# Optimization experiments

Measured on AMD Instinct MI355X. Metric: run time of the kernel, lower is better.

The kernel has to match this reference:

```python
import jax, jax.numpy as jnp
import numpy as np

T, K, E, H, I = 2048, 8, 32, 1024, 768


def setup_inputs() -> dict:
    key = jax.random.key(0)
    k0, k1, k2, k3, k4, k5 = jax.random.split(key, 6)
    sh = 1.0 / np.sqrt(H).astype(np.float32)
    si = 1.0 / np.sqrt(I).astype(np.float32)
    return {
        "hidden_states": jax.random.normal(k0, (T, H), jnp.float32),
        "top_k_index": jax.random.randint(k1, (T, K), 0, E),
        "top_k_weights": jax.random.uniform(k2, (T, K), jnp.float32),
        "gate_proj": jax.random.normal(k3, (E, I, H), jnp.float32) * sh,
        "up_proj": jax.random.normal(k4, (E, I, H), jnp.float32) * sh,
        "down_proj": jax.random.normal(k5, (E, H, I), jnp.float32) * si,
    }


def reference(hidden_states, top_k_index, top_k_weights, gate_proj, up_proj, down_proj):
    # Tokens not routed to expert e get combine weight 0, so summing the
    # weighted per-expert outputs over all experts reproduces the original
    # gather -> SwiGLU MLP -> scale -> index_add_ exactly (duplicated expert
    # hits within a token's top-k sum, matching repeated index_add_).
    n_tok = hidden_states.shape[0]
    n_exp = gate_proj.shape[0]
    combine = jnp.zeros((n_tok, n_exp), hidden_states.dtype)
    combine = combine.at[jnp.arange(n_tok)[:, None], top_k_index].add(top_k_weights)

    def body(acc, xs):
        g_w, u_w, d_w, w_e = xs  # g_w,u_w: [I,H]; d_w: [H,I]; w_e: [T]
        h = jax.nn.silu(hidden_states @ g_w.T) * (hidden_states @ u_w.T)  # [T,I]
        y = h @ d_w.T  # [T,H]
        return acc + y * w_e[:, None], None

    out, _ = jax.lax.scan(
        body,
        jnp.zeros_like(hidden_states),
        (gate_proj, up_proj, down_proj, combine.T),
    )
    return out
```

## Files before the change

### kernel.cpp

```cpp
#include <hip/hip_runtime.h>

#define T_TOK 2048
#define TOPK  8
#define NEXP  32
#define HDIM  1024
#define IDIM  768
#define NPAIR (T_TOK * TOPK)
#define BM 128
#define BK 32
#define MT_MAX (NPAIR / BM + NEXP)

typedef __attribute__((ext_vector_type(8))) short short8;
typedef __attribute__((ext_vector_type(4))) float f32x4;

__device__ __forceinline__ unsigned short f2bf(float f) {
    unsigned x = __float_as_uint(f);
    unsigned r = x + 0x7fffu + ((x >> 16) & 1u);
    return (unsigned short)(r >> 16);
}
__device__ __forceinline__ float bf2f(unsigned short u) {
    return __uint_as_float(((unsigned)u) << 16);
}

__device__ __forceinline__ void gl_lds16(const unsigned short* g, void* l) {
    __builtin_amdgcn_global_load_lds((const __attribute__((address_space(1))) void*)g,
                                     (__attribute__((address_space(3))) void*)l, 16, 0, 0);
}

__device__ __forceinline__ int mt_swz(int bx) {
    return ((bx >> 4) << 4) | ((bx & 7) << 1) | ((bx >> 3) & 1);
}

#define VMCNT(n) asm volatile("s_waitcnt vmcnt(" #n ")" ::: "memory")
#define BARRIER  __builtin_amdgcn_s_barrier()

__global__ void k_conv2(const float* __restrict__ src0, const float* __restrict__ src1,
                        unsigned short* __restrict__ dst, int n4each) {
    int i = blockIdx.x * 256 + threadIdx.x;
    const float* s = (i < n4each) ? src0 : src1;
    int j = (i < n4each) ? i : i - n4each;
    if (i < 2 * n4each) {
        float4 v = ((const float4*)s)[j];
        ushort4 o;
        o.x = f2bf(v.x); o.y = f2bf(v.y); o.z = f2bf(v.z); o.w = f2bf(v.w);
        ((ushort4*)dst)[i] = o;
    }
}

__global__ void k_conv(const float* __restrict__ src, unsigned short* __restrict__ dst, int n4) {
    int i = blockIdx.x * 256 + threadIdx.x;
    if (i < n4) {
        float4 v = ((const float4*)src)[i];
        ushort4 o;
        o.x = f2bf(v.x); o.y = f2bf(v.y); o.z = f2bf(v.z); o.w = f2bf(v.w);
        ((ushort4*)dst)[i] = o;
    }
}

__global__ void k_init(int* counts) {
    if (threadIdx.x < NEXP) counts[threadIdx.x] = 0;
}

__global__ void k_hist(const int* __restrict__ idx, int* __restrict__ counts) {
    int p = blockIdx.x * 256 + threadIdx.x;
    atomicAdd(&counts[idx[p]], 1);
}

__global__ void k_scan(const int* __restrict__ counts, int* __restrict__ offsets,
                       int* __restrict__ mtb, int* __restrict__ cursor) {
    if (threadIdx.x == 0) {
        int tot = 0, mt = 0;
        for (int e = 0; e < NEXP; ++e) {
            offsets[e] = tot; mtb[e] = mt;
            tot += counts[e];
            mt += (counts[e] + BM - 1) / BM;
        }
        offsets[NEXP] = tot; mtb[NEXP] = mt;
    }
    if (threadIdx.x < NEXP) cursor[threadIdx.x] = 0;
}

__global__ void k_scatter(const int* __restrict__ idx, int* __restrict__ cursor,
                          const int* __restrict__ offsets, int* __restrict__ pair_token,
                          int* __restrict__ pair_slot) {
    int p = blockIdx.x * 256 + threadIdx.x;
    int e = idx[p];
    int pos = atomicAdd(&cursor[e], 1);
    int slot = offsets[e] + pos;
    pair_token[slot] = p >> 3;
    pair_slot[p] = slot;
}

__global__ __launch_bounds__(256, 2) void k_gateup(
    const unsigned short* __restrict__ hid_bf, const unsigned short* __restrict__ gate_bf,
    const unsigned short* __restrict__ up_bf, const int* __restrict__ pair_token,
    const int* __restrict__ offsets, const int* __restrict__ mtb,
    unsigned short* __restrict__ h_mid)
{
    __shared__ short8 sBuf[2][1536];
    __shared__ int sInfo[4];
    int tid = threadIdx.x;
    int mt = mt_swz(blockIdx.x);
    if (tid == 0 && mt >= mtb[NEXP]) sInfo[0] = -1;
    if (tid < NEXP) {
        int lo = mtb[tid], hi = mtb[tid + 1];
        if (lo <= mt && mt < hi) {
            sInfo[0] = tid; sInfo[1] = offsets[tid];
            sInfo[2] = offsets[tid + 1] - offsets[tid];
            sInfo[3] = (mt - lo) * BM;
        }
    }
    __syncthreads();
    int e = sInfo[0];
    if (e < 0) return;
    int off = sInfo[1], Me = sInfo[2], mrow0 = sInfo[3];
    int n0 = blockIdx.y * 128;

    int wave = tid >> 6, lane = tid & 63, quad = lane >> 4, l16 = lane & 15;

    int m0 = wave * 32 + l16, m1 = m0 + 16;
    int rp0 = mrow0 + m0, rp1 = mrow0 + m1;
    int tok0 = (rp0 < Me) ? pair_token[off + rp0] : 0;
    int tok1 = (rp1 < Me) ? pair_token[off + rp1] : 0;
    const unsigned short* aG0 = hid_bf + (size_t)tok0 * HDIM + quad * 8;
    const unsigned short* aG1 = hid_bf + (size_t)tok1 * HDIM + quad * 8;
    const unsigned short* gG0 = gate_bf + ((size_t)e * IDIM + n0 + m0) * HDIM + quad * 8;
    const unsigned short* gG1 = gate_bf + ((size_t)e * IDIM + n0 + m1) * HDIM + quad * 8;
    const unsigned short* uG0 = up_bf + ((size_t)e * IDIM + n0 + m0) * HDIM + quad * 8;
    const unsigned short* uG1 = up_bf + ((size_t)e * IDIM + n0 + m1) * HDIM + quad * 8;
    const int dA = wave * 128;
    const int dG = 512 + wave * 128;
    const int dU = 1024 + wave * 128;

    int wm = (wave & 1) * 64, wn = (wave >> 1) * 64;
    int aBase = (wm >> 4) * 64 + quad * 16 + l16;
    int bBase = (wn >> 4) * 64 + quad * 16 + l16;

    f32x4 zero = {0.f, 0.f, 0.f, 0.f};
    f32x4 accg[4][4], accu[4][4];
#pragma unroll
    for (int i = 0; i < 4; ++i)
#pragma unroll
        for (int j = 0; j < 4; ++j) { accg[i][j] = zero; accu[i][j] = zero; }

#define STAGE_GU(b, k0) do { \
        short8* nb_ = &sBuf[b][0]; \
        gl_lds16(aG0 + (k0), (void*)(nb_ + dA));      gl_lds16(aG1 + (k0), (void*)(nb_ + dA + 64)); \
        gl_lds16(gG0 + (k0), (void*)(nb_ + dG));      gl_lds16(gG1 + (k0), (void*)(nb_ + dG + 64)); \
        gl_lds16(uG0 + (k0), (void*)(nb_ + dU));      gl_lds16(uG1 + (k0), (void*)(nb_ + dU + 64)); \
    } while (0)

#define COMP_GU(b) do { \
        const short8* cb_ = &sBuf[b][0]; \
        short8 af_[4]; \
        _Pragma("unroll") for (int fm = 0; fm < 4; ++fm) af_[fm] = cb_[aBase + fm * 64]; \
        _Pragma("unroll") for (int fn = 0; fn < 4; ++fn) { \
            short8 bg_ = cb_[512 + bBase + fn * 64]; \
            short8 bu_ = cb_[1024 + bBase + fn * 64]; \
            _Pragma("unroll") for (int fm = 0; fm < 4; ++fm) { \
                accg[fm][fn] = __builtin_amdgcn_mfma_f32_16x16x32_bf16(af_[fm], bg_, accg[fm][fn], 0, 0, 0); \
                accu[fm][fn] = __builtin_amdgcn_mfma_f32_16x16x32_bf16(af_[fm], bu_, accu[fm][fn], 0, 0, 0); \
            } \
        } \
    } while (0)

    STAGE_GU(0, 0);
    STAGE_GU(1, BK);
#pragma unroll 1
    for (int tt = 0; tt < HDIM / BK - 2; tt += 2) {
        VMCNT(6); BARRIER; COMP_GU(0); BARRIER; STAGE_GU(0, (tt + 2) * BK);
        VMCNT(6); BARRIER; COMP_GU(1); BARRIER; STAGE_GU(1, (tt + 3) * BK);
    }
    VMCNT(6); BARRIER; COMP_GU(0);
    VMCNT(0); BARRIER; COMP_GU(1);

#pragma unroll
    for (int fm = 0; fm < 4; ++fm)
#pragma unroll
        for (int fn = 0; fn < 4; ++fn)
#pragma unroll
            for (int r = 0; r < 4; ++r) {
                int mloc = wm + fm * 16 + quad * 4 + r;
                int prow = mrow0 + mloc;
                if (prow < Me) {
                    int col = n0 + wn + fn * 16 + l16;
                    float g = accg[fm][fn][r], u = accu[fm][fn][r];
                    float h = g / (1.f + __expf(-g)) * u;
                    h_mid[(size_t)(off + prow) * IDIM + col] = f2bf(h);
                }
            }
}

__global__ __launch_bounds__(256, 2) void k_down(
    const unsigned short* __restrict__ h_mid, const unsigned short* __restrict__ down_bf,
    const int* __restrict__ offsets, const int* __restrict__ mtb,
    unsigned short* __restrict__ y_pair)
{
    __shared__ short8 sBuf[2][1536];
    __shared__ int sInfo[4];
    int tid = threadIdx.x;
    int mt = mt_swz(blockIdx.x);
    if (tid == 0 && mt >= mtb[NEXP]) sInfo[0] = -1;
    if (tid < NEXP) {
        int lo = mtb[tid], hi = mtb[tid + 1];
        if (lo <= mt && mt < hi) {
            sInfo[0] = tid; sInfo[1] = offsets[tid];
            sInfo[2] = offsets[tid + 1] - offsets[tid];
            sInfo[3] = (mt - lo) * BM;
        }
    }
    __syncthreads();
    int e = sInfo[0];
    if (e < 0) return;
    int off = sInfo[1], Me = sInfo[2], mrow0 = sInfo[3];
    int n0 = blockIdx.y * 256;

    int wave = tid >> 6, lane = tid & 63, quad = lane >> 4, l16 = lane & 15;

    int m0 = wave * 32 + l16, m1 = m0 + 16;
    int rp0 = mrow0 + m0; if (rp0 >= Me) rp0 = 0;
    int rp1 = mrow0 + m1; if (rp1 >= Me) rp1 = 0;
    const unsigned short* aG0 = h_mid + (size_t)(off + rp0) * IDIM + quad * 8;
    const unsigned short* aG1 = h_mid + (size_t)(off + rp1) * IDIM + quad * 8;
    const unsigned short* bG0 = down_bf + ((size_t)e * HDIM + n0 + wave * 64 + l16) * IDIM + quad * 8;
    const unsigned short* bG1 = bG0 + (size_t)16 * IDIM;
    const unsigned short* bG2 = bG0 + (size_t)32 * IDIM;
    const unsigned short* bG3 = bG0 + (size_t)48 * IDIM;
    const int dA = wave * 128;
    const int dB = 512 + wave * 256;

    int wm = (wave & 1) * 64, wn = (wave >> 1) * 128;
    int aBase = (wm >> 4) * 64 + quad * 16 + l16;
    int bBase = (wn >> 4) * 64 + quad * 16 + l16;

    f32x4 zero = {0.f, 0.f, 0.f, 0.f};
    f32x4 acc[4][8];
#pragma unroll
    for (int i = 0; i < 4; ++i)
#pragma unroll
        for (int j = 0; j < 8; ++j) acc[i][j] = zero;

#define STAGE_DN(b, k0) do { \
        short8* nb_ = &sBuf[b][0]; \
        gl_lds16(aG0 + (k0), (void*)(nb_ + dA));       gl_lds16(aG1 + (k0), (void*)(nb_ + dA + 64)); \
        gl_lds16(bG0 + (k0), (void*)(nb_ + dB));       gl_lds16(bG1 + (k0), (void*)(nb_ + dB + 64)); \
        gl_lds16(bG2 + (k0), (void*)(nb_ + dB + 128)); gl_lds16(bG3 + (k0), (void*)(nb_ + dB + 192)); \
    } while (0)

#define COMP_DN(b) do { \
        const short8* cb_ = &sBuf[b][0]; \
        short8 af_[4]; \
        _Pragma("unroll") for (int fm = 0; fm < 4; ++fm) af_[fm] = cb_[aBase + fm * 64]; \
        _Pragma("unroll") for (int fn = 0; fn < 8; ++fn) { \
            short8 bb_ = cb_[512 + bBase + fn * 64]; \
            _Pragma("unroll") for (int fm = 0; fm < 4; ++fm) \
                acc[fm][fn] = __builtin_amdgcn_mfma_f32_16x16x32_bf16(af_[fm], bb_, acc[fm][fn], 0, 0, 0); \
        } \
    } while (0)

    STAGE_DN(0, 0);
    STAGE_DN(1, BK);
#pragma unroll 1
    for (int tt = 0; tt < IDIM / BK - 2; tt += 2) {
        VMCNT(6); BARRIER; COMP_DN(0); BARRIER; STAGE_DN(0, (tt + 2) * BK);
        VMCNT(6); BARRIER; COMP_DN(1); BARRIER; STAGE_DN(1, (tt + 3) * BK);
    }
    VMCNT(6); BARRIER; COMP_DN(0);
    VMCNT(0); BARRIER; COMP_DN(1);

#pragma unroll
    for (int fm = 0; fm < 4; ++fm)
#pragma unroll
        for (int fn = 0; fn < 8; ++fn)
#pragma unroll
            for (int r = 0; r < 4; ++r) {
                int mloc = wm + fm * 16 + quad * 4 + r;
                int prow = mrow0 + mloc;
                if (prow < Me) {
                    int col = n0 + wn + fn * 16 + l16;
                    y_pair[(size_t)(off + prow) * HDIM + col] = f2bf(acc[fm][fn][r]);
                }
            }
}

__global__ void k_reduce(const unsigned short* __restrict__ y_pair,
                         const int* __restrict__ pair_slot,
                         const float* __restrict__ topw, float* __restrict__ out)
{
    int t = blockIdx.x;
    __shared__ int ss[TOPK];
    __shared__ float sw[TOPK];
    if (threadIdx.x < TOPK) {
        ss[threadIdx.x] = pair_slot[t * TOPK + threadIdx.x];
        sw[threadIdx.x] = topw[t * TOPK + threadIdx.x];
    }
    __syncthreads();
    int c = threadIdx.x * 4;
    float a0 = 0.f, a1 = 0.f, a2 = 0.f, a3 = 0.f;
    for (int k = 0; k < TOPK; ++k) {
        const unsigned short* yr = y_pair + (size_t)ss[k] * HDIM + c;
        uint2 v = *(const uint2*)yr;
        float w = sw[k];
        a0 += w * bf2f((unsigned short)(v.x & 0xffff));
        a1 += w * bf2f((unsigned short)(v.x >> 16));
        a2 += w * bf2f((unsigned short)(v.y & 0xffff));
        a3 += w * bf2f((unsigned short)(v.y >> 16));
    }
    float4 o = {a0, a1, a2, a3};
    *(float4*)(out + (size_t)t * HDIM + c) = o;
}

extern "C" void kernel_launch(void* const* d_in, const int* in_sizes, int n_in,
                              void* d_out, int out_size, void* d_ws, size_t ws_size,
                              hipStream_t stream) {
    (void)in_sizes; (void)n_in; (void)out_size; (void)ws_size;
    const float* hidden = (const float*)d_in[0];
    const int*   tki    = (const int*)d_in[1];
    const float* tkw    = (const float*)d_in[2];
    const float* gate   = (const float*)d_in[3];
    const float* up     = (const float*)d_in[4];
    const float* down   = (const float*)d_in[5];
    float* out = (float*)d_out;

    char* w = (char*)d_ws;
    unsigned short* h_mid   = (unsigned short*)w;
    unsigned short* hid_bf  = (unsigned short*)(w + 25165824);
    unsigned short* gate_bf = (unsigned short*)(w + 29360128);
    unsigned short* up_bf   = (unsigned short*)(w + 79691776);
    unsigned short* down_bf = gate_bf;
    unsigned short* y_pair  = up_bf;
    int* ib = (int*)(w + 130023424);
    int* pair_token = ib;
    int* pair_slot  = ib + NPAIR;
    int* counts     = ib + 2 * NPAIR;
    int* cursor     = counts + NEXP;
    int* offsets    = cursor + NEXP;
    int* mtb        = offsets + NEXP + 1;

    const int W4 = NEXP * IDIM * HDIM / 4;
    const int H4 = T_TOK * HDIM / 4;

    k_init<<<1, 64, 0, stream>>>(counts);
    k_hist<<<NPAIR / 256, 256, 0, stream>>>(tki, counts);
    k_scan<<<1, 64, 0, stream>>>(counts, offsets, mtb, cursor);
    k_scatter<<<NPAIR / 256, 256, 0, stream>>>(tki, cursor, offsets, pair_token, pair_slot);

    k_conv<<<(H4 + 255) / 256, 256, 0, stream>>>(hidden, hid_bf, H4);
    k_conv2<<<(2 * W4 + 255) / 256, 256, 0, stream>>>(gate, up, gate_bf, W4);

    k_gateup<<<dim3(MT_MAX, IDIM / 128), 256, 0, stream>>>(hid_bf, gate_bf, up_bf,
                                                           pair_token, offsets, mtb, h_mid);

    k_conv<<<(W4 + 255) / 256, 256, 0, stream>>>(down, down_bf, W4);

    k_down<<<dim3(MT_MAX, HDIM / 256), 256, 0, stream>>>(h_mid, down_bf, offsets, mtb, y_pair);
    k_reduce<<<T_TOK, 256, 0, stream>>>(y_pair, pair_slot, tkw, out);
}
```

Before: 545.5 us.

## Drop LDS staging in MoE GEMMs; load MFMA fragments directly from global

Both grouped GEMM kernels stop staging tiles through shared memory with global_load_lds and barriers. Each wave now loads its own bf16 fragments straight from global memory into registers with a two-slot register double buffer. The output tiles are halved (gate/up 128x64, down 128x128) and occupancy is raised to 3 blocks per SIMD group. This removes LDS traffic and barrier stalls, but each wave now loads its own copy of tiles that were shared in LDS, so global and L2 traffic goes up and the 16-byte-per-lane loads are less coalesced.

```diff
diff --git a/kernel.cpp b/kernel.cpp
--- a/kernel.cpp
+++ b/kernel.cpp
@@ -22,17 +22,9 @@
     return __uint_as_float(((unsigned)u) << 16);
 }
 
-__device__ __forceinline__ void gl_lds16(const unsigned short* g, void* l) {
-    __builtin_amdgcn_global_load_lds((const __attribute__((address_space(1))) void*)g,
-                                     (__attribute__((address_space(3))) void*)l, 16, 0, 0);
-}
-
 __device__ __forceinline__ int mt_swz(int bx) {
     return ((bx >> 4) << 4) | ((bx & 7) << 1) | ((bx >> 3) & 1);
 }
-
-#define VMCNT(n) asm volatile("s_waitcnt vmcnt(" #n ")" ::: "memory")
-#define BARRIER  __builtin_amdgcn_s_barrier()
 
 __global__ void k_conv2(const float* __restrict__ src0, const float* __restrict__ src1,
                         unsigned short* __restrict__ dst, int n4each) {
@@ -91,13 +83,12 @@
     pair_slot[p] = slot;
 }
 
-__global__ __launch_bounds__(256, 2) void k_gateup(
+__global__ __launch_bounds__(256, 3) void k_gateup(
     const unsigned short* __restrict__ hid_bf, const unsigned short* __restrict__ gate_bf,
     const unsigned short* __restrict__ up_bf, const int* __restrict__ pair_token,
     const int* __restrict__ offsets, const int* __restrict__ mtb,
     unsigned short* __restrict__ h_mid)
 {
-    __shared__ short8 sBuf[2][1536];
     __shared__ int sInfo[4];
     int tid = threadIdx.x;
     int mt = mt_swz(blockIdx.x);
@@ -114,70 +105,66 @@
     int e = sInfo[0];
     if (e < 0) return;
     int off = sInfo[1], Me = sInfo[2], mrow0 = sInfo[3];
-    int n0 = blockIdx.y * 128;
+    int n0 = blockIdx.y * 64;
 
     int wave = tid >> 6, lane = tid & 63, quad = lane >> 4, l16 = lane & 15;
-
-    int m0 = wave * 32 + l16, m1 = m0 + 16;
-    int rp0 = mrow0 + m0, rp1 = mrow0 + m1;
-    int tok0 = (rp0 < Me) ? pair_token[off + rp0] : 0;
-    int tok1 = (rp1 < Me) ? pair_token[off + rp1] : 0;
-    const unsigned short* aG0 = hid_bf + (size_t)tok0 * HDIM + quad * 8;
-    const unsigned short* aG1 = hid_bf + (size_t)tok1 * HDIM + quad * 8;
-    const unsigned short* gG0 = gate_bf + ((size_t)e * IDIM + n0 + m0) * HDIM + quad * 8;
-    const unsigned short* gG1 = gate_bf + ((size_t)e * IDIM + n0 + m1) * HDIM + quad * 8;
-    const unsigned short* uG0 = up_bf + ((size_t)e * IDIM + n0 + m0) * HDIM + quad * 8;
-    const unsigned short* uG1 = up_bf + ((size_t)e * IDIM + n0 + m1) * HDIM + quad * 8;
-    const int dA = wave * 128;
-    const int dG = 512 + wave * 128;
-    const int dU = 1024 + wave * 128;
-
-    int wm = (wave & 1) * 64, wn = (wave >> 1) * 64;
-    int aBase = (wm >> 4) * 64 + quad * 16 + l16;
-    int bBase = (wn >> 4) * 64 + quad * 16 + l16;
+    int wm = (wave & 1) * 64, wn = (wave >> 1) * 32;
+
+    const unsigned short* aP[4];
+#pragma unroll
+    for (int fm = 0; fm < 4; ++fm) {
+        int rp = mrow0 + wm + fm * 16 + l16;
+        int tok = pair_token[off + ((rp < Me) ? rp : (Me - 1))];
+        aP[fm] = hid_bf + (size_t)tok * HDIM + quad * 8;
+    }
+    const unsigned short* gP[2];
+    const unsigned short* uP[2];
+#pragma unroll
+    for (int fn = 0; fn < 2; ++fn) {
+        size_t row = (size_t)e * IDIM + n0 + wn + fn * 16 + l16;
+        gP[fn] = gate_bf + row * HDIM + quad * 8;
+        uP[fn] = up_bf   + row * HDIM + quad * 8;
+    }
 
     f32x4 zero = {0.f, 0.f, 0.f, 0.f};
-    f32x4 accg[4][4], accu[4][4];
+    f32x4 accg[4][2], accu[4][2];
 #pragma unroll
     for (int i = 0; i < 4; ++i)
 #pragma unroll
-        for (int j = 0; j < 4; ++j) { accg[i][j] = zero; accu[i][j] = zero; }
-
-#define STAGE_GU(b, k0) do { \
-        short8* nb_ = &sBuf[b][0]; \
-        gl_lds16(aG0 + (k0), (void*)(nb_ + dA));      gl_lds16(aG1 + (k0), (void*)(nb_ + dA + 64)); \
-        gl_lds16(gG0 + (k0), (void*)(nb_ + dG));      gl_lds16(gG1 + (k0), (void*)(nb_ + dG + 64)); \
-        gl_lds16(uG0 + (k0), (void*)(nb_ + dU));      gl_lds16(uG1 + (k0), (void*)(nb_ + dU + 64)); \
+        for (int j = 0; j < 2; ++j) { accg[i][j] = zero; accu[i][j] = zero; }
+
+    short8 A0[4], G0[2], U0[2], A1[4], G1[2], U1[2];
+
+#define LDALL_GU(A_, G_, U_, kk) do { \
+        _Pragma("unroll") for (int i = 0; i < 4; ++i) A_[i] = *(const short8*)(aP[i] + (kk)); \
+        _Pragma("unroll") for (int i = 0; i < 2; ++i) G_[i] = *(const short8*)(gP[i] + (kk)); \
+        _Pragma("unroll") for (int i = 0; i < 2; ++i) U_[i] = *(const short8*)(uP[i] + (kk)); \
     } while (0)
 
-#define COMP_GU(b) do { \
-        const short8* cb_ = &sBuf[b][0]; \
-        short8 af_[4]; \
-        _Pragma("unroll") for (int fm = 0; fm < 4; ++fm) af_[fm] = cb_[aBase + fm * 64]; \
-        _Pragma("unroll") for (int fn = 0; fn < 4; ++fn) { \
-            short8 bg_ = cb_[512 + bBase + fn * 64]; \
-            short8 bu_ = cb_[1024 + bBase + fn * 64]; \
+#define FMA_GU(A_, G_, U_) do { \
+        _Pragma("unroll") for (int fn = 0; fn < 2; ++fn) \
             _Pragma("unroll") for (int fm = 0; fm < 4; ++fm) { \
-                accg[fm][fn] = __builtin_amdgcn_mfma_f32_16x16x32_bf16(af_[fm], bg_, accg[fm][fn], 0, 0, 0); \
-                accu[fm][fn] = __builtin_amdgcn_mfma_f32_16x16x32_bf16(af_[fm], bu_, accu[fm][fn], 0, 0, 0); \
+                accg[fm][fn] = __builtin_amdgcn_mfma_f32_16x16x32_bf16(A_[fm], G_[fn], accg[fm][fn], 0, 0, 0); \
+                accu[fm][fn] = __builtin_amdgcn_mfma_f32_16x16x32_bf16(A_[fm], U_[fn], accu[fm][fn], 0, 0, 0); \
             } \
-        } \
     } while (0)
 
-    STAGE_GU(0, 0);
-    STAGE_GU(1, BK);
+    LDALL_GU(A0, G0, U0, 0);
 #pragma unroll 1
-    for (int tt = 0; tt < HDIM / BK - 2; tt += 2) {
-        VMCNT(6); BARRIER; COMP_GU(0); BARRIER; STAGE_GU(0, (tt + 2) * BK);
-        VMCNT(6); BARRIER; COMP_GU(1); BARRIER; STAGE_GU(1, (tt + 3) * BK);
-    }
-    VMCNT(6); BARRIER; COMP_GU(0);
-    VMCNT(0); BARRIER; COMP_GU(1);
+    for (int k0 = 0; k0 < HDIM - 64; k0 += 64) {
+        LDALL_GU(A1, G1, U1, k0 + 32);
+        FMA_GU(A0, G0, U0);
+        LDALL_GU(A0, G0, U0, k0 + 64);
+        FMA_GU(A1, G1, U1);
+    }
+    LDALL_GU(A1, G1, U1, HDIM - 32);
+    FMA_GU(A0, G0, U0);
+    FMA_GU(A1, G1, U1);
 
 #pragma unroll
     for (int fm = 0; fm < 4; ++fm)
 #pragma unroll
-        for (int fn = 0; fn < 4; ++fn)
+        for (int fn = 0; fn < 2; ++fn)
 #pragma unroll
             for (int r = 0; r < 4; ++r) {
                 int mloc = wm + fm * 16 + quad * 4 + r;
@@ -191,12 +178,11 @@
             }
 }
 
-__global__ __launch_bounds__(256, 2) void k_down(
+__global__ __launch_bounds__(256, 3) void k_down(
     const unsigned short* __restrict__ h_mid, const unsigned short* __restrict__ down_bf,
     const int* __restrict__ offsets, const int* __restrict__ mtb,
     unsigned short* __restrict__ y_pair)
 {
-    __shared__ short8 sBuf[2][1536];
     __shared__ int sInfo[4];
     int tid = threadIdx.x;
     int mt = mt_swz(blockIdx.x);
@@ -213,65 +199,59 @@
     int e = sInfo[0];
     if (e < 0) return;
     int off = sInfo[1], Me = sInfo[2], mrow0 = sInfo[3];
-    int n0 = blockIdx.y * 256;
+    int n0 = blockIdx.y * 128;
 
     int wave = tid >> 6, lane = tid & 63, quad = lane >> 4, l16 = lane & 15;
-
-    int m0 = wave * 32 + l16, m1 = m0 + 16;
-    int rp0 = mrow0 + m0; if (rp0 >= Me) rp0 = 0;
-    int rp1 = mrow0 + m1; if (rp1 >= Me) rp1 = 0;
-    const unsigned short* aG0 = h_mid + (size_t)(off + rp0) * IDIM + quad * 8;
-    const unsigned short* aG1 = h_mid + (size_t)(off + rp1) * IDIM + quad * 8;
-    const unsigned short* bG0 = down_bf + ((size_t)e * HDIM + n0 + wave * 64 + l16) * IDIM + quad * 8;
-    const unsigned short* bG1 = bG0 + (size_t)16 * IDIM;
-    const unsigned short* bG2 = bG0 + (size_t)32 * IDIM;
-    const unsigned short* bG3 = bG0 + (size_t)48 * IDIM;
-    const int dA = wave * 128;
-    const int dB = 512 + wave * 256;
-
-    int wm = (wave & 1) * 64, wn = (wave >> 1) * 128;
-    int aBase = (wm >> 4) * 64 + quad * 16 + l16;
-    int bBase = (wn >> 4) * 64 + quad * 16 + l16;
+    int wm = (wave & 1) * 64, wn = (wave >> 1) * 64;
+
+    const unsigned short* aP[4];
+#pragma unroll
+    for (int fm = 0; fm < 4; ++fm) {
+        int rp = mrow0 + wm + fm * 16 + l16;
+        if (rp >= Me) rp = Me - 1;
+        aP[fm] = h_mid + (size_t)(off + rp) * IDIM + quad * 8;
+    }
+    const unsigned short* bP[4];
+#pragma unroll
+    for (int fn = 0; fn < 4; ++fn)
+        bP[fn] = down_bf + ((size_t)e * HDIM + n0 + wn + fn * 16 + l16) * IDIM + quad * 8;
 
     f32x4 zero = {0.f, 0.f, 0.f, 0.f};
-    f32x4 acc[4][8];
+    f32x4 acc[4][4];
 #pragma unroll
     for (int i = 0; i < 4; ++i)
 #pragma unroll
-        for (int j = 0; j < 8; ++j) acc[i][j] = zero;
-
-#define STAGE_DN(b, k0) do { \
-        short8* nb_ = &sBuf[b][0]; \
-        gl_lds16(aG0 + (k0), (void*)(nb_ + dA));       gl_lds16(aG1 + (k0), (void*)(nb_ + dA + 64)); \
-        gl_lds16(bG0 + (k0), (void*)(nb_ + dB));       gl_lds16(bG1 + (k0), (void*)(nb_ + dB + 64)); \
-        gl_lds16(bG2 + (k0), (void*)(nb_ + dB + 128)); gl_lds16(bG3 + (k0), (void*)(nb_ + dB + 192)); \
+        for (int j = 0; j < 4; ++j) acc[i][j] = zero;
+
+    short8 A0[4], B0[4], A1[4], B1[4];
+
+#define LDALL_DN(A_, B_, kk) do { \
+        _Pragma("unroll") for (int i = 0; i < 4; ++i) A_[i] = *(const short8*)(aP[i] + (kk)); \
+        _Pragma("unroll") for (int i = 0; i < 4; ++i) B_[i] = *(const short8*)(bP[i] + (kk)); \
     } while (0)
 
-#define COMP_DN(b) do { \
-        const short8* cb_ = &sBuf[b][0]; \
-        short8 af_[4]; \
-        _Pragma("unroll") for (int fm = 0; fm < 4; ++fm) af_[fm] = cb_[aBase + fm * 64]; \
-        _Pragma("unroll") for (int fn = 0; fn < 8; ++fn) { \
-            short8 bb_ = cb_[512 + bBase + fn * 64]; \
+#define FMA_DN(A_, B_) do { \
+        _Pragma("unroll") for (int fn = 0; fn < 4; ++fn) \
             _Pragma("unroll") for (int fm = 0; fm < 4; ++fm) \
-                acc[fm][fn] = __builtin_amdgcn_mfma_f32_16x16x32_bf16(af_[fm], bb_, acc[fm][fn], 0, 0, 0); \
-        } \
+                acc[fm][fn] = __builtin_amdgcn_mfma_f32_16x16x32_bf16(A_[fm], B_[fn], acc[fm][fn], 0, 0, 0); \
     } while (0)
 
-    STAGE_DN(0, 0);
-    STAGE_DN(1, BK);
+    LDALL_DN(A0, B0, 0);
 #pragma unroll 1
-    for (int tt = 0; tt < IDIM / BK - 2; tt += 2) {
-        VMCNT(6); BARRIER; COMP_DN(0); BARRIER; STAGE_DN(0, (tt + 2) * BK);
-        VMCNT(6); BARRIER; COMP_DN(1); BARRIER; STAGE_DN(1, (tt + 3) * BK);
-    }
-    VMCNT(6); BARRIER; COMP_DN(0);
-    VMCNT(0); BARRIER; COMP_DN(1);
+    for (int k0 = 0; k0 < IDIM - 64; k0 += 64) {
+        LDALL_DN(A1, B1, k0 + 32);
+        FMA_DN(A0, B0);
+        LDALL_DN(A0, B0, k0 + 64);
+        FMA_DN(A1, B1);
+    }
+    LDALL_DN(A1, B1, IDIM - 32);
+    FMA_DN(A0, B0);
+    FMA_DN(A1, B1);
 
 #pragma unroll
     for (int fm = 0; fm < 4; ++fm)
 #pragma unroll
-        for (int fn = 0; fn < 8; ++fn)
+        for (int fn = 0; fn < 4; ++fn)
 #pragma unroll
             for (int r = 0; r < 4; ++r) {
                 int mloc = wm + fm * 16 + quad * 4 + r;
@@ -348,11 +328,11 @@
     k_conv<<<(H4 + 255) / 256, 256, 0, stream>>>(hidden, hid_bf, H4);
     k_conv2<<<(2 * W4 + 255) / 256, 256, 0, stream>>>(gate, up, gate_bf, W4);
 
-    k_gateup<<<dim3(MT_MAX, IDIM / 128), 256, 0, stream>>>(hid_bf, gate_bf, up_bf,
-                                                           pair_token, offsets, mtb, h_mid);
+    k_gateup<<<dim3(MT_MAX, IDIM / 64), 256, 0, stream>>>(hid_bf, gate_bf, up_bf,
+                                                          pair_token, offsets, mtb, h_mid);
 
     k_conv<<<(W4 + 255) / 256, 256, 0, stream>>>(down, down_bf, W4);
 
-    k_down<<<dim3(MT_MAX, HDIM / 256), 256, 0, stream>>>(h_mid, down_bf, offsets, mtb, y_pair);
+    k_down<<<dim3(MT_MAX, HDIM / 128), 256, 0, stream>>>(h_mid, down_bf, offsets, mtb, y_pair);
     k_reduce<<<T_TOK, 256, 0, stream>>>(y_pair, pair_slot, tkw, out);
 }
```

New measurement: 722.5 us. 32.5% more time.
